# Kernel optimization log

Hardware: AMD Instinct MI355X
Metric: run time of the kernel (lower is better)

The kernel has to match this reference:

```python
import jax, jax.numpy as jnp
import numpy as np

BASE = 7.0  # ModularPhaseNorm modulus


def _plane_rotate(x, theta):
    # Rotate the first 2*P dims of x in P independent 2D planes by learned angles theta [P].
    P = theta.shape[0]
    c, s = jnp.cos(theta), jnp.sin(theta)  # [P]
    head = x[..., : 2 * P].reshape(x.shape[:-1] + (P, 2))
    a, b = head[..., 0], head[..., 1]
    rot = jnp.stack([c * a - s * b, s * a + c * b], axis=-1)
    rot = rot.reshape(x.shape[:-1] + (2 * P,))
    return jnp.concatenate([rot, x[..., 2 * P :]], axis=-1)


def _modular_phase_norm(x, gamma, beta, base=BASE):
    # Wrap activations into [-base/2, base/2) (modular phase), then affine per-channel.
    wrapped = x - base * jnp.floor(x / base + 0.5)
    return gamma * wrapped + beta


def setup_inputs() -> dict:
    key = jax.random.key(0)
    ks = jax.random.split(key, 8)
    B, F, T, H = 8192, 4096, 9, 32
    team_paths = jax.random.normal(ks[0], (B, F, T), dtype=jnp.float32)
    W1 = jax.random.normal(ks[1], (F, H), dtype=jnp.float32) / np.sqrt(F)
    b1 = jnp.zeros((H,), dtype=jnp.float32)
    theta1 = jax.random.normal(ks[2], (2,), dtype=jnp.float32)  # num_rotation_planes=2
    gamma = jnp.ones((H,), dtype=jnp.float32)
    beta = jnp.zeros((H,), dtype=jnp.float32)
    W2 = jax.random.normal(ks[3], (H, 1), dtype=jnp.float32) / np.sqrt(H)
    b2 = jnp.zeros((1,), dtype=jnp.float32)
    theta2 = jax.random.normal(ks[4], (2,), dtype=jnp.float32)
    return {"team_paths": team_paths, "theta1": theta1, "W1": W1, "b1": b1,
            "gamma": gamma, "beta": beta, "theta2": theta2, "W2": W2, "b2": b2}


def reference(team_paths, theta1, W1, b1, gamma, beta, theta2, W2, b2):
    # Batch the per-member Python loop: [B, F, T] -> [B, T, F]
    x = jnp.transpose(team_paths, (0, 2, 1))
    # eidosTransform(feature_dim -> 32, 2 rotation planes)
    h = _plane_rotate(x, theta1)
    h = jnp.einsum("btf,fh->bth", h, W1) + b1
    # ModularPhaseNorm(32, base=7)
    h = _modular_phase_norm(h, gamma, beta)
    # eidosTransform(32 -> 1, 2 rotation planes)
    h = _plane_rotate(h, theta2)
    scores = jnp.einsum("bth,ho->bto", h, W2)[..., 0] + b2[0]  # [B, T]
    return jax.nn.softmax(scores, axis=1)
```

## Files before the change

### kernel.cpp

```cpp
#include <hip/hip_runtime.h>
#include <math.h>

typedef float f2v __attribute__((ext_vector_type(2)));
typedef float f4v __attribute__((ext_vector_type(4)));

#define TF 256
#define NTILE 16
#define FT 36864

__global__ __launch_bounds__(256) void scorer_kernel(
    const float* __restrict__ x,
    const float* __restrict__ th1,
    const float* __restrict__ W1,
    const float* __restrict__ b1,
    const float* __restrict__ gamma,
    const float* __restrict__ beta,
    const float* __restrict__ th2,
    const float* __restrict__ W2,
    const float* __restrict__ b2p,
    float* __restrict__ out)
{
    __shared__ __align__(16) float xl[2 * TF * 9];
    const int tid = threadIdx.x;
    const int b0 = blockIdx.x * 2;
    const int hg = tid & 7;
    const int fc = tid >> 3;
    const float* xb = x + (size_t)b0 * FT;

    float acc[2][9][4];
    #pragma unroll
    for (int b = 0; b < 2; ++b)
        #pragma unroll
        for (int t = 0; t < 9; ++t)
            #pragma unroll
            for (int j = 0; j < 4; ++j) acc[b][t][j] = 0.f;

    const f4v* __restrict__ W1v = (const f4v*)W1;

    for (int tile = 0; tile < NTILE; ++tile) {
        const int fbase = tile * TF;
        __syncthreads();
        const f2v* s0 = (const f2v*)(xb + fbase * 9);
        const f2v* s1 = (const f2v*)(xb + FT + fbase * 9);
        f2v* dst = (f2v*)xl;
        #pragma unroll
        for (int k = 0; k < 9; ++k) {
            int s = tid + k * 256;
            f2v v;
            if (s < 1152) v = __builtin_nontemporal_load(&s0[s]);
            else          v = __builtin_nontemporal_load(&s1[s - 1152]);
            dst[s] = v;
        }
        __syncthreads();
        if (tile == 0) {
            if (tid < 36) {
                int bb = tid / 18, r = tid % 18, t = r >> 1, p = r & 1;
                float c = cosf(th1[p]), sn = sinf(th1[p]);
                float a  = xl[bb * 2304 + (2 * p) * 9 + t];
                float bv = xl[bb * 2304 + (2 * p + 1) * 9 + t];
                xl[bb * 2304 + (2 * p) * 9 + t]     = c * a - sn * bv;
                xl[bb * 2304 + (2 * p + 1) * 9 + t] = sn * a + c * bv;
            }
            __syncthreads();
        }
        const int f0 = fbase + fc * 8;
        #pragma unroll
        for (int i = 0; i < 8; ++i) {
            const f4v w = W1v[(size_t)(f0 + i) * 8 + hg];
            const float* xp = &xl[(fc * 8 + i) * 9];
            #pragma unroll
            for (int t = 0; t < 9; ++t) {
                float xv0 = xp[t];
                float xv1 = xp[t + 2304];
                acc[0][t][0] += xv0 * w.x;
                acc[0][t][1] += xv0 * w.y;
                acc[0][t][2] += xv0 * w.z;
                acc[0][t][3] += xv0 * w.w;
                acc[1][t][0] += xv1 * w.x;
                acc[1][t][1] += xv1 * w.y;
                acc[1][t][2] += xv1 * w.z;
                acc[1][t][3] += xv1 * w.w;
            }
        }
    }

    __syncthreads();

    float* af = (float*)acc;
    #pragma unroll
    for (int q = 0; q < 72; ++q) {
        float v = af[q];
        v += __shfl_xor(v, 8);
        v += __shfl_xor(v, 16);
        v += __shfl_xor(v, 32);
        af[q] = v;
    }
    const int wv = tid >> 6;
    const int lane = tid & 63;
    if (lane < 8) {
        float* dstp = &xl[(wv * 8 + lane) * 72];
        #pragma unroll
        for (int q = 0; q < 72; ++q) dstp[q] = af[q];
    }
    __syncthreads();

    for (int o = tid; o < 576; o += 256) {
        int h = o & 31;
        int t = (o >> 5) % 9;
        int bb = o / 288;
        int hg2 = h >> 2, j = h & 3;
        int idx = bb * 36 + t * 4 + j;
        float v = xl[(0 * 8 + hg2) * 72 + idx]
                + xl[(1 * 8 + hg2) * 72 + idx]
                + xl[(2 * 8 + hg2) * 72 + idx]
                + xl[(3 * 8 + hg2) * 72 + idx];
        v += b1[h];
        float wr = v - 7.0f * floorf(v / 7.0f + 0.5f);
        float g = gamma[h] * wr + beta[h];
        xl[2304 + bb * 288 + t * 32 + h] = g;
    }
    __syncthreads();

    if (tid < 18) {
        int bb = tid / 9, t = tid % 9;
        const float* g = &xl[2304 + bb * 288 + t * 32];
        float c0 = cosf(th2[0]), s0r = sinf(th2[0]);
        float c1 = cosf(th2[1]), s1r = sinf(th2[1]);
        float sc = (c0 * g[0] - s0r * g[1]) * W2[0]
                 + (s0r * g[0] + c0 * g[1]) * W2[1]
                 + (c1 * g[2] - s1r * g[3]) * W2[2]
                 + (s1r * g[2] + c1 * g[3]) * W2[3];
        #pragma unroll
        for (int h = 4; h < 32; ++h) sc += g[h] * W2[h];
        sc += b2p[0];
        xl[2880 + bb * 9 + t] = sc;
    }
    __syncthreads();

    if (tid < 18) {
        int bb = tid / 9, t = tid % 9;
        const float* sb = &xl[2880 + bb * 9];
        float m = sb[0];
        #pragma unroll
        for (int k = 1; k < 9; ++k) m = fmaxf(m, sb[k]);
        float den = 0.f;
        #pragma unroll
        for (int k = 0; k < 9; ++k) den += expf(sb[k] - m);
        out[(size_t)(b0 + bb) * 9 + t] = expf(sb[t] - m) / den;
    }
}

extern "C" void kernel_launch(void* const* d_in, const int* in_sizes, int n_in,
                              void* d_out, int out_size, void* d_ws, size_t ws_size,
                              hipStream_t stream) {
    const float* x     = (const float*)d_in[0];
    const float* th1   = (const float*)d_in[1];
    const float* W1    = (const float*)d_in[2];
    const float* b1    = (const float*)d_in[3];
    const float* gamma = (const float*)d_in[4];
    const float* beta  = (const float*)d_in[5];
    const float* th2   = (const float*)d_in[6];
    const float* W2    = (const float*)d_in[7];
    const float* b2    = (const float*)d_in[8];
    float* out = (float*)d_out;

    const int B = in_sizes[0] / FT;
    dim3 grid(B / 2), block(256);
    hipLaunchKernelGGL(scorer_kernel, grid, block, 0, stream,
                       x, th1, W1, b1, gamma, beta, th2, W2, b2, out);
}
```

Measured before the change: 395.2 us.

## Register-prefetch next x tile, pack FMAs, and interleave W1 rows

Loads the next feature tile of x into registers while the current tile is computed from shared memory, so global-load latency overlaps compute. Accumulators become float2 vectors to allow packed FMA instructions. W1 rows are software-prefetched one step ahead, and the feature row mapping changes from contiguous blocks of 8 per thread to a stride of 32, which changes the LDS access pattern. It also adds an occupancy hint of 4 blocks per CU, at the risk of register pressure and spills from the 18 extra prefetch registers.

```diff
diff --git a/kernel.cpp b/kernel.cpp
--- a/kernel.cpp
+++ b/kernel.cpp
@@ -8,7 +8,7 @@
 #define NTILE 16
 #define FT 36864
 
-__global__ __launch_bounds__(256) void scorer_kernel(
+__global__ __launch_bounds__(256, 4) void scorer_kernel(
     const float* __restrict__ x,
     const float* __restrict__ th1,
     const float* __restrict__ W1,
@@ -27,31 +27,41 @@
     const int fc = tid >> 3;
     const float* xb = x + (size_t)b0 * FT;
 
-    float acc[2][9][4];
+    f2v acc[2][9][2];
     #pragma unroll
     for (int b = 0; b < 2; ++b)
         #pragma unroll
         for (int t = 0; t < 9; ++t)
             #pragma unroll
-            for (int j = 0; j < 4; ++j) acc[b][t][j] = 0.f;
+            for (int jv = 0; jv < 2; ++jv) { acc[b][t][jv].x = 0.f; acc[b][t][jv].y = 0.f; }
 
     const f4v* __restrict__ W1v = (const f4v*)W1;
 
+    f2v pre[9];
+    #pragma unroll
+    for (int k = 0; k < 9; ++k) {
+        int s = tid + k * 256;
+        const f2v* sp = (s < 1152) ? ((const f2v*)xb) + s
+                                   : ((const f2v*)(xb + FT)) + (s - 1152);
+        pre[k] = __builtin_nontemporal_load(sp);
+    }
+
     for (int tile = 0; tile < NTILE; ++tile) {
-        const int fbase = tile * TF;
         __syncthreads();
-        const f2v* s0 = (const f2v*)(xb + fbase * 9);
-        const f2v* s1 = (const f2v*)(xb + FT + fbase * 9);
         f2v* dst = (f2v*)xl;
         #pragma unroll
-        for (int k = 0; k < 9; ++k) {
-            int s = tid + k * 256;
-            f2v v;
-            if (s < 1152) v = __builtin_nontemporal_load(&s0[s]);
-            else          v = __builtin_nontemporal_load(&s1[s - 1152]);
-            dst[s] = v;
+        for (int k = 0; k < 9; ++k) dst[tid + k * 256] = pre[k];
+        __syncthreads();
+        if (tile + 1 < NTILE) {
+            const int off = (tile + 1) * 1152;
+            #pragma unroll
+            for (int k = 0; k < 9; ++k) {
+                int s = tid + k * 256;
+                const f2v* sp = (s < 1152) ? ((const f2v*)xb) + off + s
+                                           : ((const f2v*)(xb + FT)) + off + (s - 1152);
+                pre[k] = __builtin_nontemporal_load(sp);
+            }
         }
-        __syncthreads();
         if (tile == 0) {
             if (tid < 36) {
                 int bb = tid / 18, r = tid % 18, t = r >> 1, p = r & 1;
@@ -63,45 +73,51 @@
             }
             __syncthreads();
         }
-        const int f0 = fbase + fc * 8;
+        const int fbase = tile * TF;
+        f4v w = W1v[(size_t)(fbase + fc) * 8 + hg];
         #pragma unroll
         for (int i = 0; i < 8; ++i) {
-            const f4v w = W1v[(size_t)(f0 + i) * 8 + hg];
-            const float* xp = &xl[(fc * 8 + i) * 9];
+            const int row = i * 32 + fc;
+            f4v wn = w;
+            if (i < 7) wn = W1v[(size_t)(fbase + row + 32) * 8 + hg];
+            f2v wlo = {w.x, w.y}, whi = {w.z, w.w};
+            const float* xp0 = &xl[row * 9];
+            const float* xp1 = xp0 + 2304;
             #pragma unroll
             for (int t = 0; t < 9; ++t) {
-                float xv0 = xp[t];
-                float xv1 = xp[t + 2304];
-                acc[0][t][0] += xv0 * w.x;
-                acc[0][t][1] += xv0 * w.y;
-                acc[0][t][2] += xv0 * w.z;
-                acc[0][t][3] += xv0 * w.w;
-                acc[1][t][0] += xv1 * w.x;
-                acc[1][t][1] += xv1 * w.y;
-                acc[1][t][2] += xv1 * w.z;
-                acc[1][t][3] += xv1 * w.w;
+                float s0 = xp0[t], s1 = xp1[t];
+                f2v x0 = {s0, s0};
+                f2v x1 = {s1, s1};
+                acc[0][t][0] += x0 * wlo;
+                acc[0][t][1] += x0 * whi;
+                acc[1][t][0] += x1 * wlo;
+                acc[1][t][1] += x1 * whi;
             }
+            w = wn;
         }
     }
 
     __syncthreads();
 
-    float* af = (float*)acc;
-    #pragma unroll
-    for (int q = 0; q < 72; ++q) {
-        float v = af[q];
-        v += __shfl_xor(v, 8);
-        v += __shfl_xor(v, 16);
-        v += __shfl_xor(v, 32);
-        af[q] = v;
-    }
     const int wv = tid >> 6;
     const int lane = tid & 63;
-    if (lane < 8) {
-        float* dstp = &xl[(wv * 8 + lane) * 72];
+    float* redbase = &xl[(wv * 8 + lane) * 72];
+    #pragma unroll
+    for (int b = 0; b < 2; ++b)
         #pragma unroll
-        for (int q = 0; q < 72; ++q) dstp[q] = af[q];
-    }
+        for (int t = 0; t < 9; ++t)
+            #pragma unroll
+            for (int jv = 0; jv < 2; ++jv) {
+                f2v v = acc[b][t][jv];
+                v.x += __shfl_xor(v.x, 8);  v.y += __shfl_xor(v.y, 8);
+                v.x += __shfl_xor(v.x, 16); v.y += __shfl_xor(v.y, 16);
+                v.x += __shfl_xor(v.x, 32); v.y += __shfl_xor(v.y, 32);
+                if (lane < 8) {
+                    int idx = b * 36 + t * 4 + jv * 2;
+                    redbase[idx]     = v.x;
+                    redbase[idx + 1] = v.y;
+                }
+            }
     __syncthreads();
 
     for (int o = tid; o < 576; o += 256) {
```

Measured after the change: 815.7 us. 106% more time.
